# Optimization experiments

Measured on AMD Instinct MI355X. Metric: run time of the kernel, lower is better.

## Reference

```python
import jax, jax.numpy as jnp
import numpy as np

B, S, D, H, DH, BS, L, R, V, FF = 4, 4096, 768, 12, 64, 64, 2, 3, 50257, 3072
NB = S // BS          # 64 key/query blocks
NSEL = 5 + R          # 2 global + 3 window + R random key blocks per query block


def layer_norm(x, g, b, eps=1e-12):
    m = jnp.mean(x, axis=-1, keepdims=True)
    v = jnp.mean(jnp.square(x - m), axis=-1, keepdims=True)
    return (x - m) * jax.lax.rsqrt(v + eps) * g + b


def setup_inputs() -> dict:
    key = jax.random.key(0)
    ks = iter(jax.random.split(key, 16))
    p = lambda shape: jax.random.normal(next(ks), shape, jnp.float32) * 0.02
    return {
        'input_ids': jax.random.randint(next(ks), (B, S), 0, V, jnp.int32),
        'attention_mask': jnp.ones((B, S), jnp.int32),
        'label': jax.random.randint(next(ks), (B,), 0, 2, jnp.int32),
        'rand_idx': jax.random.randint(next(ks), (NB, R), 0, NB, jnp.int32),
        'emb': p((V, D)), 'pos_emb': p((S, D)),
        'ln_emb_g': jnp.ones((D,)), 'ln_emb_b': jnp.zeros((D,)),
        'Wqkv': p((L, D, 3 * D)), 'bqkv': jnp.zeros((L, 3 * D)),
        'Wo': p((L, D, D)), 'bo': jnp.zeros((L, D)),
        'ln1_g': jnp.ones((L, D)), 'ln1_b': jnp.zeros((L, D)),
        'Wff1': p((L, D, FF)), 'bff1': jnp.zeros((L, FF)),
        'Wff2': p((L, FF, D)), 'bff2': jnp.zeros((L, D)),
        'ln2_g': jnp.ones((L, D)), 'ln2_b': jnp.zeros((L, D)),
        'Wp': p((D, D)), 'bp': jnp.zeros((D,)),
        'Wc': p((D, 2)), 'bc': jnp.zeros((2,)),
    }


def reference(input_ids, attention_mask, label, rand_idx, emb, pos_emb,
              ln_emb_g, ln_emb_b, Wqkv, bqkv, Wo, bo, ln1_g, ln1_b,
              Wff1, bff1, Wff2, bff2, ln2_g, ln2_b, Wp, bp, Wc, bc):
    blk = jnp.arange(NB, dtype=jnp.int32)
    sel = jnp.concatenate([
        jnp.zeros((NB, 1), jnp.int32),
        ((blk - 1) % NB)[:, None], blk[:, None], ((blk + 1) % NB)[:, None],
        jnp.full((NB, 1), NB - 1, jnp.int32),
        rand_idx.astype(jnp.int32),
    ], axis=1)  # [NB, NSEL]

    h = emb[input_ids] + pos_emb[None]                 # [B,S,D]
    h = layer_norm(h, ln_emb_g, ln_emb_b)

    mblk = attention_mask.reshape(B, NB, BS)
    mask_sel = mblk[:, sel].reshape(B, 1, NB, 1, NSEL * BS)  # gathered key mask
    bias = jnp.where(mask_sel > 0, 0.0, -1e9).astype(h.dtype)

    scale = 1.0 / np.sqrt(DH)
    for l in range(L):
        qkv = h @ Wqkv[l] + bqkv[l]
        q, k, v = jnp.split(qkv, 3, axis=-1)
        to_blocks = lambda t: t.reshape(B, NB, BS, H, DH).transpose(0, 3, 1, 2, 4)  # [B,H,NB,BS,DH]
        qb, kb, vb = to_blocks(q), to_blocks(k), to_blocks(v)
        ksel = kb[:, :, sel].reshape(B, H, NB, NSEL * BS, DH)  # gather sparse key blocks
        vsel = vb[:, :, sel].reshape(B, H, NB, NSEL * BS, DH)
        scores = jnp.einsum('bhnqd,bhnkd->bhnqk', qb, ksel) * scale + bias
        attn = jax.nn.softmax(scores, axis=-1)
        ob = jnp.einsum('bhnqk,bhnkd->bhnqd', attn, vsel)
        o = ob.transpose(0, 2, 3, 1, 4).reshape(B, S, D)
        h = layer_norm(h + o @ Wo[l] + bo[l], ln1_g[l], ln1_b[l])
        ff = jax.nn.gelu(h @ Wff1[l] + bff1[l]) @ Wff2[l] + bff2[l]
        h = layer_norm(h + ff, ln2_g[l], ln2_b[l])

    pooled = jnp.tanh(h[:, 0] @ Wp + bp)               # BERT-style pooler on [CLS]
    probs = jax.nn.softmax(pooled @ Wc + bc, axis=1)
    # Faithful to the original: CrossEntropyLoss applied to softmax OUTPUT (double softmax)
    loss = -jnp.mean(jax.nn.log_softmax(probs, axis=1)[jnp.arange(B), label])
    return probs, loss
```

## Files before the change

kernel.cpp:

```cpp
#include <hip/hip_runtime.h>
#include <hip/hip_bf16.h>
#include <stdint.h>


using bf16 = __hip_bfloat16;
typedef __bf16 bf16x8 __attribute__((ext_vector_type(8)));
typedef __bf16 bf16x4 __attribute__((ext_vector_type(4)));
typedef float f32x4 __attribute__((ext_vector_type(4)));

__device__ __forceinline__ float b2f(bf16 x) { return __bfloat162float(x); }
__device__ __forceinline__ bf16 f2b(float x) { return __float2bfloat16(x); }
__device__ __forceinline__ __bf16 f2br(float x) {
  bf16 h = __float2bfloat16(x);
  return *reinterpret_cast<__bf16*>(&h);
}
__device__ __forceinline__ float ldf(const void* p, size_t i, int flag) {
  return flag ? __bfloat162float(((const bf16*)p)[i]) : ((const float*)p)[i];
}

__device__ __forceinline__ void gld_lds16(const bf16* g, bf16* l) {
  __builtin_amdgcn_global_load_lds((__attribute__((address_space(1))) void*)g,
                                   (__attribute__((address_space(3))) void*)l, 16, 0, 0);
}

__device__ __forceinline__ f32x4 mfma16(bf16x8 a, bf16x8 b, f32x4 c) {
  return __builtin_amdgcn_mfma_f32_16x16x32_bf16(a, b, c, 0, 0, 0);
}

__device__ __forceinline__ float gelu_f(float x) {
  const float z = 1.5957691216057308f * (x + 0.044715f * x * x * x);
  return x / (1.0f + __expf(-z));
}

__global__ void probe_kernel(const uint32_t* __restrict__ g, int* __restrict__ flag) {
  if (threadIdx.x == 0) flag[0] = (g[0] == 0x3F803F80u) ? 1 : 0;
}

__global__ __launch_bounds__(256) void transpose_k(const void* __restrict__ in, size_t in_off,
                                                   bf16* __restrict__ out, int K, int N,
                                                   const int* __restrict__ dflag) {
  __shared__ float tile[32][33];
  const int flag = dflag[0];
  const int bx = blockIdx.x * 32;
  const int by = blockIdx.y * 32;
  const int tx = threadIdx.x & 31, ty = threadIdx.x >> 5;
#pragma unroll
  for (int i = 0; i < 32; i += 8)
    tile[ty + i][tx] = ldf(in, in_off + (size_t)(by + ty + i) * N + bx + tx, flag);
  __syncthreads();
#pragma unroll
  for (int i = 0; i < 32; i += 8)
    out[(size_t)(bx + ty + i) * K + by + tx] = f2b(tile[tx][ty + i]);
}

__global__ __launch_bounds__(256) void embed_ln_kernel(
    const int* __restrict__ ids, const void* __restrict__ emb, const void* __restrict__ pos,
    const void* __restrict__ g, const void* __restrict__ bb, bf16* __restrict__ h,
    const int* __restrict__ dflag) {
  __shared__ float red[8];
  const int flag = dflag[0];
  const int tok = blockIdx.x;
  const int tid = threadIdx.x;
  const int s = tok & 4095;
  const size_t id = (size_t)ids[tok];
  float v[3]; float sum = 0.f, sq = 0.f;
#pragma unroll
  for (int i = 0; i < 3; i++) {
    const int d = tid + i * 256;
    v[i] = ldf(emb, id * 768 + d, flag) + ldf(pos, (size_t)s * 768 + d, flag);
    sum += v[i]; sq += v[i] * v[i];
  }
#pragma unroll
  for (int off = 32; off >= 1; off >>= 1) { sum += __shfl_down(sum, off); sq += __shfl_down(sq, off); }
  if ((tid & 63) == 0) { red[(tid >> 6) * 2] = sum; red[(tid >> 6) * 2 + 1] = sq; }
  __syncthreads();
  sum = red[0] + red[2] + red[4] + red[6];
  sq  = red[1] + red[3] + red[5] + red[7];
  const float mean = sum * (1.0f / 768.0f);
  const float var = sq * (1.0f / 768.0f) - mean * mean;
  const float rs = rsqrtf(var + 1e-12f);
  bf16* hr = h + (size_t)tok * 768;
#pragma unroll
  for (int i = 0; i < 3; i++) {
    const int d = tid + i * 256;
    hr[d] = f2b((v[i] - mean) * rs * ldf(g, d, flag) + ldf(bb, d, flag));
  }
}

__global__ __launch_bounds__(256) void add_ln_kernel(
    bf16* __restrict__ h, const bf16* __restrict__ x,
    const void* __restrict__ g, const void* __restrict__ bb, size_t goff,
    const int* __restrict__ dflag) {
  __shared__ float red[8];
  const int flag = dflag[0];
  const int tok = blockIdx.x;
  const int tid = threadIdx.x;
  const size_t base = (size_t)tok * 768;
  float v[3]; float sum = 0.f, sq = 0.f;
#pragma unroll
  for (int i = 0; i < 3; i++) {
    const int d = tid + i * 256;
    v[i] = b2f(h[base + d]) + b2f(x[base + d]);
    sum += v[i]; sq += v[i] * v[i];
  }
#pragma unroll
  for (int off = 32; off >= 1; off >>= 1) { sum += __shfl_down(sum, off); sq += __shfl_down(sq, off); }
  if ((tid & 63) == 0) { red[(tid >> 6) * 2] = sum; red[(tid >> 6) * 2 + 1] = sq; }
  __syncthreads();
  sum = red[0] + red[2] + red[4] + red[6];
  sq  = red[1] + red[3] + red[5] + red[7];
  const float mean = sum * (1.0f / 768.0f);
  const float var = sq * (1.0f / 768.0f) - mean * mean;
  const float rs = rsqrtf(var + 1e-12f);
#pragma unroll
  for (int i = 0; i < 3; i++) {
    const int d = tid + i * 256;
    h[base + d] = f2b((v[i] - mean) * rs * ldf(g, goff + d, flag) + ldf(bb, goff + d, flag));
  }
}

template <int EPI, bool ABLK>
__global__ __launch_bounds__(256) void gemm_bt(
    const bf16* __restrict__ A, const bf16* __restrict__ Bt,
    const void* __restrict__ bias, size_t bias_off, bf16* __restrict__ C,
    int N, int K,
    bf16* __restrict__ qout, bf16* __restrict__ kout, bf16* __restrict__ vout,
    const int* __restrict__ dflag) {
  __shared__ __align__(16) bf16 smem[9216];
  bf16* sA = smem;
  bf16* sB = smem + 4096;
  const int m0 = blockIdx.x * 128;
  const int n0 = blockIdx.y * 128;
  const int tid = threadIdx.x;
  const int lane = tid & 63;
  const int wv = tid >> 6;
  const int wm = wv >> 1, wn = wv & 1;
  const int col = lane & 15, quad = lane >> 4;

  f32x4 acc[4][4] = {};

  const int sr = tid >> 2;
  const int kc = ((tid & 3) - ((tid >> 4) & 3)) & 3;
  const int sc = kc * 8;
  const bf16* gA = A + (size_t)(m0 + sr) * K + sc;
  const bf16* gB = Bt + (size_t)(n0 + sr) * K + sc;
  const size_t rstep = (size_t)64 * K;

  size_t cb0 = 0, cb1 = 0;
  if constexpr (ABLK) {
    const int t0 = m0 + sr, t1 = t0 + 64;
    cb0 = (size_t)(t0 >> 12) * 3145728 + ((t0 >> 6) & 63) * 4096 + (t0 & 63) * 64;
    cb1 = (size_t)(t1 >> 12) * 3145728 + ((t1 >> 6) & 63) * 4096 + (t1 & 63) * 64;
  }

  const int sl = (quad + (col >> 2)) & 3;

  for (int k0 = 0; k0 < K; k0 += 32) {
    const bf16 *pA0, *pA1;
    if constexpr (ABLK) {
      const int c = k0 + sc;
      const int hh = c >> 6, dh = c & 63;
      pA0 = A + cb0 + hh * 262144 + dh;
      pA1 = A + cb1 + hh * 262144 + dh;
    } else {
      pA0 = gA; pA1 = gA + rstep; gA += 32;
    }
    gld_lds16(pA0, sA + tid * 8);
    gld_lds16(pA1, sA + 2048 + tid * 8);
    gld_lds16(gB, sB + tid * 8);
    gld_lds16(gB + rstep, sB + 2048 + tid * 8);
    gB += 32;
    __syncthreads();
    bf16x8 av[4], bv[4];
#pragma unroll
    for (int t = 0; t < 4; t++)
      av[t] = *(const bf16x8*)(sA + (wm * 64 + t * 16 + col) * 32 + sl * 8);
#pragma unroll
    for (int t = 0; t < 4; t++)
      bv[t] = *(const bf16x8*)(sB + (wn * 64 + t * 16 + col) * 32 + sl * 8);
#pragma unroll
    for (int mt = 0; mt < 4; mt++)
#pragma unroll
      for (int nt = 0; nt < 4; nt++)
        acc[mt][nt] = mfma16(av[mt], bv[nt], acc[mt][nt]);
    __syncthreads();
  }

  const int flag = dflag[0];
  float bsv[4];
#pragma unroll
  for (int nt = 0; nt < 4; nt++)
    bsv[nt] = ldf(bias, bias_off + n0 + wn * 64 + nt * 16 + col, flag);

  if constexpr (EPI != 2) {
    for (int half = 0; half < 2; half++) {
      __syncthreads();
      if (wm == half) {
#pragma unroll
        for (int nt = 0; nt < 4; nt++)
#pragma unroll
          for (int mt = 0; mt < 4; mt++)
#pragma unroll
            for (int r = 0; r < 4; r++) {
              float val = acc[mt][nt][r] + bsv[nt];
              if constexpr (EPI == 1) val = gelu_f(val);
              smem[(mt * 16 + quad * 4 + r) * 136 + wn * 64 + nt * 16 + col] = f2b(val);
            }
      }
      __syncthreads();
#pragma unroll
      for (int rr = 0; rr < 4; rr++) {
        const int row = rr * 16 + (tid >> 4);
        const int ch = tid & 15;
        const bf16x8 vv = *(const bf16x8*)(smem + row * 136 + ch * 8);
        *(bf16x8*)(C + (size_t)(m0 + half * 64 + row) * N + n0 + ch * 8) = vv;
      }
    }
  } else {
    const int part = (n0 >= 1536) ? 2 : ((n0 >= 768) ? 1 : 0);
    const int w0 = n0 - part * 768;
    const int h0 = w0 >> 6;
    const int bb = m0 >> 12;
    for (int half = 0; half < 2; half++) {
      const int nb_ = ((m0 >> 6) & 63) + half;
      __syncthreads();
      if (wm == half) {
        if (part < 2) {
#pragma unroll
          for (int nt = 0; nt < 4; nt++)
#pragma unroll
            for (int mt = 0; mt < 4; mt++)
#pragma unroll
              for (int r = 0; r < 4; r++)
                smem[(mt * 16 + quad * 4 + r) * 136 + wn * 64 + nt * 16 + col] =
                    f2b(acc[mt][nt][r] + bsv[nt]);
        } else {
#pragma unroll
          for (int nt = 0; nt < 4; nt++) {
            const int ncol = wn * 64 + nt * 16 + col;
#pragma unroll
            for (int mt = 0; mt < 4; mt++) {
              bf16x4 pk;
#pragma unroll
              for (int r = 0; r < 4; r++) pk[r] = f2br(acc[mt][nt][r] + bsv[nt]);
              *(bf16x4*)(smem + ncol * 72 + mt * 16 + quad * 4) = pk;
            }
          }
        }
      }
      __syncthreads();
      const int j = tid >> 7;
      const size_t dbase = (size_t)((bb * 12 + h0 + j) * 64 + nb_) * 4096;
      if (part < 2) {
        bf16* dst = (part == 0) ? qout : kout;
#pragma unroll
        for (int rr = 0; rr < 4; rr++) {
          const int tsk = (tid & 127) + rr * 128;
          const int row = tsk >> 3, pc = tsk & 7;
          const bf16x8 vv = *(const bf16x8*)(smem + row * 136 + j * 64 + pc * 8);
          *(bf16x8*)(dst + dbase + row * 64 + pc * 8) = vv;
        }
      } else {
#pragma unroll
        for (int rr = 0; rr < 4; rr++) {
          const int tsk = (tid & 127) + rr * 128;
          const int dh = tsk >> 3, pc = tsk & 7;
          const bf16x8 vv = *(const bf16x8*)(smem + (j * 64 + dh) * 72 + pc * 8);
          *(bf16x8*)(vout + dbase + dh * 64 + pc * 8) = vv;
        }
      }
    }
  }
}

__global__ __launch_bounds__(256, 4) void attn_kernel(
    const bf16* q, const bf16* __restrict__ kmat, const bf16* __restrict__ vT,
    const int* __restrict__ amask, const int* __restrict__ rand_idx, bf16* o) {
  __shared__ __align__(16) bf16 sK[2][4096];
  __shared__ __align__(16) bf16 sV[2][4096];
  const int idx = blockIdx.x;
  const int nb = idx & 63;
  const int bh = idx >> 6;
  const int bb = bh / 12;
  const int tid = threadIdx.x;
  const int wv = tid >> 6, lane = tid & 63;
  const int col = lane & 15, quad = lane >> 4;

  int sel[8];
  sel[0] = 0; sel[1] = (nb + 63) & 63; sel[2] = nb; sel[3] = (nb + 1) & 63;
  sel[4] = 63;
  sel[5] = rand_idx[nb * 3 + 0];
  sel[6] = rand_idx[nb * 3 + 1];
  sel[7] = rand_idx[nb * 3 + 2];

  const size_t bhbase = (size_t)bh * 64;

  const bf16* qb = q + (bhbase + nb) * 4096;
  const int qrow = wv * 16 + col;
  const bf16x8 bq0 = *(const bf16x8*)(qb + qrow * 64 + quad * 8);
  const bf16x8 bq1 = *(const bf16x8*)(qb + qrow * 64 + 32 + quad * 8);

  unsigned long long bal[8];
#pragma unroll
  for (int sb = 0; sb < 8; sb++)
    bal[sb] = __ballot(amask[bb * 4096 + sel[sb] * 64 + lane] > 0);

  const int srow = tid >> 3, sslot = tid & 7;
  const int sw0 = ((sslot ^ (srow & 7)) << 3);

  auto stage = [&](int buf, int blk) {
    const bf16* gk = kmat + (bhbase + blk) * 4096;
    const bf16* gv = vT + (bhbase + blk) * 4096;
    bf16* dk = sK[buf];
    bf16* dv = sV[buf];
    gld_lds16(gk + srow * 64 + sw0, dk + tid * 8);
    gld_lds16(gk + (srow + 32) * 64 + sw0, dk + 2048 + tid * 8);
    gld_lds16(gv + srow * 64 + sw0, dv + tid * 8);
    gld_lds16(gv + (srow + 32) * 64 + sw0, dv + 2048 + tid * 8);
  };

  f32x4 oacc[4] = {};
  float mrun = -1e30f, lrun = 0.0f;

  stage(0, sel[0]);

#pragma unroll
  for (int sb = 0; sb < 8; sb++) {
    const int cur = sb & 1;
    if (sb < 7) {
      stage(cur ^ 1, sel[sb + 1]);
      asm volatile("s_waitcnt vmcnt(4)" ::: "memory");
    } else {
      asm volatile("s_waitcnt vmcnt(0)" ::: "memory");
    }
    __builtin_amdgcn_s_barrier();
    asm volatile("" ::: "memory");

    const bf16* kb = sK[cur];
    f32x4 t[4];
#pragma unroll
    for (int c = 0; c < 4; c++) {
      const int r = c * 16 + col;
      const bf16x8 ak0 = *(const bf16x8*)(kb + r * 64 + ((quad ^ (r & 7)) << 3));
      const bf16x8 ak1 = *(const bf16x8*)(kb + r * 64 + (((4 + quad) ^ (r & 7)) << 3));
      f32x4 s4 = {};
      s4 = mfma16(ak0, bq0, s4);
      s4 = mfma16(ak1, bq1, s4);
      t[c] = s4;
    }
#pragma unroll
    for (int c = 0; c < 4; c++)
#pragma unroll
      for (int r = 0; r < 4; r++) t[c][r] *= 0.125f;
    if (bal[sb] != ~0ull) {
#pragma unroll
      for (int c = 0; c < 4; c++)
#pragma unroll
        for (int r = 0; r < 4; r++)
          if (!((bal[sb] >> (c * 16 + quad * 4 + r)) & 1)) t[c][r] -= 1e9f;
    }

    float pm = t[0][0];
#pragma unroll
    for (int c = 0; c < 4; c++)
#pragma unroll
      for (int r = 0; r < 4; r++) pm = fmaxf(pm, t[c][r]);
    pm = fmaxf(pm, __shfl_xor(pm, 16));
    pm = fmaxf(pm, __shfl_xor(pm, 32));

    const float mnew = fmaxf(mrun, pm);
    const float scale = __expf(mrun - mnew);
    float ps = 0.0f;
    bf16x8 pa8[2];
#pragma unroll
    for (int c = 0; c < 4; c++)
#pragma unroll
      for (int r = 0; r < 4; r++) {
        const float p = __expf(t[c][r] - mnew);
        ps += p;
        pa8[c >> 1][(c & 1) * 4 + r] = f2br(p);
      }
    ps += __shfl_xor(ps, 16);
    ps += __shfl_xor(ps, 32);
    lrun = lrun * scale + ps;
    mrun = mnew;

    float sc[4];
#pragma unroll
    for (int r = 0; r < 4; r++) sc[r] = __shfl(scale, quad * 4 + r);
#pragma unroll
    for (int nt = 0; nt < 4; nt++)
#pragma unroll
      for (int r = 0; r < 4; r++) oacc[nt][r] *= sc[r];

    const bf16* vb = sV[cur];
#pragma unroll
    for (int pr = 0; pr < 2; pr++) {
      const int g0 = 4 * pr + (quad >> 1);
      const int g1 = g0 + 2;
      const int so = (quad & 1) * 4;
#pragma unroll
      for (int nt = 0; nt < 4; nt++) {
        const int dh = nt * 16 + col;
        const bf16x4 bv0 = *(const bf16x4*)(vb + dh * 64 + ((g0 ^ (col & 7)) << 3) + so);
        const bf16x4 bv1 = *(const bf16x4*)(vb + dh * 64 + ((g1 ^ (col & 7)) << 3) + so);
        const bf16x8 bv8 = __builtin_shufflevector(bv0, bv1, 0, 1, 2, 3, 4, 5, 6, 7);
        oacc[nt] = mfma16(pa8[pr], bv8, oacc[nt]);
      }
    }
    asm volatile("" ::: "memory");
    __builtin_amdgcn_s_barrier();
  }

  const float invl = 1.0f / lrun;
  float iv[4];
#pragma unroll
  for (int r = 0; r < 4; r++) iv[r] = __shfl(invl, quad * 4 + r);
  bf16* ob = o + (bhbase + nb) * 4096;
#pragma unroll
  for (int nt = 0; nt < 4; nt++)
#pragma unroll
    for (int r = 0; r < 4; r++)
      ob[(wv * 16 + quad * 4 + r) * 64 + nt * 16 + col] = f2b(oacc[nt][r] * iv[r]);
}

__global__ __launch_bounds__(768) void pooler_kernel(
    const bf16* __restrict__ h, const void* __restrict__ Wp,
    const void* __restrict__ bp, float* __restrict__ pooled,
    const int* __restrict__ dflag) {
  __shared__ float hrow[768];
  const int flag = dflag[0];
  const int bb = blockIdx.x;
  const int j = threadIdx.x;
  hrow[j] = b2f(h[(size_t)bb * 4096 * 768 + j]);
  __syncthreads();
  float acc = 0.0f;
#pragma unroll 8
  for (int d = 0; d < 768; d++) acc += hrow[d] * ldf(Wp, (size_t)d * 768 + j, flag);
  pooled[bb * 768 + j] = tanhf(acc + ldf(bp, j, flag));
}

__global__ __launch_bounds__(256) void cls_kernel(
    const float* __restrict__ pooled, const void* __restrict__ Wc, const void* __restrict__ bc,
    const int* __restrict__ label, void* __restrict__ out, const int* __restrict__ dflag) {
  __shared__ float lsum[8];
  const int flag = dflag[0];
  const int tid = threadIdx.x;
  const int p = tid >> 5, i = tid & 31;
  const int bb = p >> 1, c = p & 1;
  float acc = 0.0f;
  for (int d = i; d < 768; d += 32) acc += pooled[bb * 768 + d] * ldf(Wc, (size_t)d * 2 + c, flag);
#pragma unroll
  for (int off = 16; off >= 1; off >>= 1) acc += __shfl_xor(acc, off);
  if (i == 0) lsum[p] = acc;
  __syncthreads();
  if (tid == 0) {
    float res[9];
    float loss = 0.0f;
    for (int b = 0; b < 4; b++) {
      const float l0 = lsum[b * 2 + 0] + ldf(bc, 0, flag);
      const float l1 = lsum[b * 2 + 1] + ldf(bc, 1, flag);
      const float m = fmaxf(l0, l1);
      const float e0 = expf(l0 - m), e1 = expf(l1 - m);
      const float s = e0 + e1;
      const float p0 = e0 / s, p1 = e1 / s;
      res[b * 2] = p0; res[b * 2 + 1] = p1;
      const float mm = fmaxf(p0, p1);
      const float lse = mm + logf(expf(p0 - mm) + expf(p1 - mm));
      const float chosen = (label[b] == 0) ? p0 : p1;
      loss -= (chosen - lse);
    }
    res[8] = loss * 0.25f;
    if (flag) { bf16* o = (bf16*)out; for (int j = 0; j < 9; j++) o[j] = f2b(res[j]); }
    else      { float* o = (float*)out; for (int j = 0; j < 9; j++) o[j] = res[j]; }
  }
}

extern "C" void kernel_launch(void* const* d_in, const int* in_sizes, int n_in,
                              void* d_out, int out_size, void* d_ws, size_t ws_size,
                              hipStream_t stream) {
  const int* input_ids      = (const int*)d_in[0];
  const int* attention_mask = (const int*)d_in[1];
  const int* label          = (const int*)d_in[2];
  const int* rand_idx       = (const int*)d_in[3];
  const void* emb      = d_in[4];
  const void* pos_emb  = d_in[5];
  const void* ln_emb_g = d_in[6];
  const void* ln_emb_b = d_in[7];
  const void* Wqkv = d_in[8];
  const void* bqkv = d_in[9];
  const void* Wo   = d_in[10];
  const void* bo   = d_in[11];
  const void* ln1_g = d_in[12];
  const void* ln1_b = d_in[13];
  const void* Wff1 = d_in[14];
  const void* bff1 = d_in[15];
  const void* Wff2 = d_in[16];
  const void* bff2 = d_in[17];
  const void* ln2_g = d_in[18];
  const void* ln2_b = d_in[19];
  const void* Wp = d_in[20];
  const void* bp = d_in[21];
  const void* Wc = d_in[22];
  const void* bc = d_in[23];

  bf16* ws = (bf16*)d_ws;
  size_t off = 0;
  int* dflag = (int*)(ws + off); off += 8;
  bf16* WqkvT = ws + off; off += (size_t)2 * 2304 * 768;
  bf16* WoT   = ws + off; off += (size_t)2 * 768 * 768;
  bf16* Wff1T = ws + off; off += (size_t)2 * 3072 * 768;
  bf16* Wff2T = ws + off; off += (size_t)2 * 768 * 3072;
  bf16* hbuf  = ws + off; off += (size_t)16384 * 768;
  bf16* qo    = ws + off; off += (size_t)16384 * 768;
  bf16* kbf   = ws + off; off += (size_t)16384 * 768;
  bf16* vbf   = ws + off; off += (size_t)16384 * 768;
  bf16* xbf   = ws + off; off += (size_t)16384 * 768;
  bf16* a1buf = ws + off; off += (size_t)16384 * 3072;
  float* pooled = (float*)(ws + off); off += 6144;

  dim3 blk(256);

  probe_kernel<<<1, 64, 0, stream>>>((const uint32_t*)ln_emb_g, dflag);

  for (int l = 0; l < 2; l++) {
    transpose_k<<<dim3(72, 24), blk, 0, stream>>>(Wqkv, (size_t)l * 768 * 2304, WqkvT + (size_t)l * 2304 * 768, 768, 2304, dflag);
    transpose_k<<<dim3(24, 24), blk, 0, stream>>>(Wo, (size_t)l * 768 * 768, WoT + (size_t)l * 768 * 768, 768, 768, dflag);
    transpose_k<<<dim3(96, 24), blk, 0, stream>>>(Wff1, (size_t)l * 768 * 3072, Wff1T + (size_t)l * 3072 * 768, 768, 3072, dflag);
    transpose_k<<<dim3(24, 96), blk, 0, stream>>>(Wff2, (size_t)l * 3072 * 768, Wff2T + (size_t)l * 768 * 3072, 3072, 768, dflag);
  }

  embed_ln_kernel<<<16384, blk, 0, stream>>>(input_ids, emb, pos_emb, ln_emb_g, ln_emb_b, hbuf, dflag);

  for (int l = 0; l < 2; l++) {
    gemm_bt<2, false><<<dim3(128, 18), blk, 0, stream>>>(hbuf, WqkvT + (size_t)l * 2304 * 768, bqkv, (size_t)l * 2304,
                                                         nullptr, 2304, 768, qo, kbf, vbf, dflag);
    attn_kernel<<<3072, blk, 0, stream>>>(qo, kbf, vbf, attention_mask, rand_idx, qo);
    gemm_bt<0, true><<<dim3(128, 6), blk, 0, stream>>>(qo, WoT + (size_t)l * 768 * 768, bo, (size_t)l * 768,
                                                       xbf, 768, 768, nullptr, nullptr, nullptr, dflag);
    add_ln_kernel<<<16384, blk, 0, stream>>>(hbuf, xbf, ln1_g, ln1_b, (size_t)l * 768, dflag);
    gemm_bt<1, false><<<dim3(128, 24), blk, 0, stream>>>(hbuf, Wff1T + (size_t)l * 3072 * 768, bff1, (size_t)l * 3072,
                                                         a1buf, 3072, 768, nullptr, nullptr, nullptr, dflag);
    gemm_bt<0, false><<<dim3(128, 6), blk, 0, stream>>>(a1buf, Wff2T + (size_t)l * 768 * 3072, bff2, (size_t)l * 768,
                                                        xbf, 768, 3072, nullptr, nullptr, nullptr, dflag);
    add_ln_kernel<<<16384, blk, 0, stream>>>(hbuf, xbf, ln2_g, ln2_b, (size_t)l * 768, dflag);
  }

  pooler_kernel<<<4, dim3(768), 0, stream>>>(hbuf, Wp, bp, pooled, dflag);
  cls_kernel<<<1, blk, 0, stream>>>(pooled, Wc, bc, label, d_out, dflag);

  (void)in_sizes; (void)n_in; (void)out_size; (void)ws_size;
}
```

Measured before the change: 1.545 ms.

## Double-buffer GEMM LDS staging and make add-LayerNorm one wave per token

The GEMM main loop now keeps two LDS buffers and issues the global-to-LDS loads for the next K-slice before computing the current one. It uses partial vmcnt waits and raw barriers, so memory latency can overlap with the MFMAs. Separately, the residual-add LayerNorm kernel processes one token per wavefront with 16-byte vector loads and stores and a pure shuffle reduction, removing the shared-memory reduction and block barrier. The costs are doubled LDS per GEMM block, which may reduce occupancy, and hand-written waitcnt logic that must match the exact number of outstanding loads.

```diff
diff --git a/kernel.cpp b/kernel.cpp
--- a/kernel.cpp
+++ b/kernel.cpp
@@ -13,6 +13,9 @@
 __device__ __forceinline__ __bf16 f2br(float x) {
   bf16 h = __float2bfloat16(x);
   return *reinterpret_cast<__bf16*>(&h);
+}
+__device__ __forceinline__ float br2f(__bf16 x) {
+  bf16 t; *reinterpret_cast<__bf16*>(&t) = x; return __bfloat162float(t);
 }
 __device__ __forceinline__ float ldf(const void* p, size_t i, int flag) {
   return flag ? __bfloat162float(((const bf16*)p)[i]) : ((const float*)p)[i];
@@ -91,31 +94,51 @@
     bf16* __restrict__ h, const bf16* __restrict__ x,
     const void* __restrict__ g, const void* __restrict__ bb, size_t goff,
     const int* __restrict__ dflag) {
-  __shared__ float red[8];
   const int flag = dflag[0];
-  const int tok = blockIdx.x;
   const int tid = threadIdx.x;
+  const int wv = tid >> 6, lane = tid & 63;
+  const int tok = blockIdx.x * 4 + wv;
   const size_t base = (size_t)tok * 768;
-  float v[3]; float sum = 0.f, sq = 0.f;
-#pragma unroll
-  for (int i = 0; i < 3; i++) {
-    const int d = tid + i * 256;
-    v[i] = b2f(h[base + d]) + b2f(x[base + d]);
-    sum += v[i]; sq += v[i] * v[i];
-  }
-#pragma unroll
-  for (int off = 32; off >= 1; off >>= 1) { sum += __shfl_down(sum, off); sq += __shfl_down(sq, off); }
-  if ((tid & 63) == 0) { red[(tid >> 6) * 2] = sum; red[(tid >> 6) * 2 + 1] = sq; }
-  __syncthreads();
-  sum = red[0] + red[2] + red[4] + red[6];
-  sq  = red[1] + red[3] + red[5] + red[7];
+
+  float v[16];
+  float sum = 0.f, sq = 0.f;
+  const bf16x8 h0 = *(const bf16x8*)(h + base + lane * 8);
+  const bf16x8 x0 = *(const bf16x8*)(x + base + lane * 8);
+#pragma unroll
+  for (int j = 0; j < 8; j++) {
+    const float t = br2f(h0[j]) + br2f(x0[j]);
+    v[j] = t; sum += t; sq += t * t;
+  }
+  if (lane < 32) {
+    const bf16x8 h1 = *(const bf16x8*)(h + base + 512 + lane * 8);
+    const bf16x8 x1 = *(const bf16x8*)(x + base + 512 + lane * 8);
+#pragma unroll
+    for (int j = 0; j < 8; j++) {
+      const float t = br2f(h1[j]) + br2f(x1[j]);
+      v[8 + j] = t; sum += t; sq += t * t;
+    }
+  }
+#pragma unroll
+  for (int off = 32; off >= 1; off >>= 1) { sum += __shfl_xor(sum, off); sq += __shfl_xor(sq, off); }
   const float mean = sum * (1.0f / 768.0f);
   const float var = sq * (1.0f / 768.0f) - mean * mean;
   const float rs = rsqrtf(var + 1e-12f);
-#pragma unroll
-  for (int i = 0; i < 3; i++) {
-    const int d = tid + i * 256;
-    h[base + d] = f2b((v[i] - mean) * rs * ldf(g, goff + d, flag) + ldf(bb, goff + d, flag));
+
+  bf16x8 o0;
+#pragma unroll
+  for (int j = 0; j < 8; j++) {
+    const int d = lane * 8 + j;
+    o0[j] = f2br((v[j] - mean) * rs * ldf(g, goff + d, flag) + ldf(bb, goff + d, flag));
+  }
+  *(bf16x8*)(h + base + lane * 8) = o0;
+  if (lane < 32) {
+    bf16x8 o1;
+#pragma unroll
+    for (int j = 0; j < 8; j++) {
+      const int d = 512 + lane * 8 + j;
+      o1[j] = f2br((v[8 + j] - mean) * rs * ldf(g, goff + d, flag) + ldf(bb, goff + d, flag));
+    }
+    *(bf16x8*)(h + base + 512 + lane * 8) = o1;
   }
 }
 
@@ -126,9 +149,7 @@
     int N, int K,
     bf16* __restrict__ qout, bf16* __restrict__ kout, bf16* __restrict__ vout,
     const int* __restrict__ dflag) {
-  __shared__ __align__(16) bf16 smem[9216];
-  bf16* sA = smem;
-  bf16* sB = smem + 4096;
+  __shared__ __align__(16) bf16 smem[16384];
   const int m0 = blockIdx.x * 128;
   const int n0 = blockIdx.y * 128;
   const int tid = threadIdx.x;
@@ -155,35 +176,55 @@
 
   const int sl = (quad + (col >> 2)) & 3;
 
-  for (int k0 = 0; k0 < K; k0 += 32) {
+  auto stage = [&](int buf, int kk) {
+    bf16* dA = smem + buf * 8192;
+    bf16* dB = dA + 4096;
     const bf16 *pA0, *pA1;
     if constexpr (ABLK) {
-      const int c = k0 + sc;
+      const int c = kk + sc;
       const int hh = c >> 6, dh = c & 63;
       pA0 = A + cb0 + hh * 262144 + dh;
       pA1 = A + cb1 + hh * 262144 + dh;
     } else {
-      pA0 = gA; pA1 = gA + rstep; gA += 32;
-    }
-    gld_lds16(pA0, sA + tid * 8);
-    gld_lds16(pA1, sA + 2048 + tid * 8);
-    gld_lds16(gB, sB + tid * 8);
-    gld_lds16(gB + rstep, sB + 2048 + tid * 8);
-    gB += 32;
-    __syncthreads();
+      pA0 = gA + kk; pA1 = gA + rstep + kk;
+    }
+    gld_lds16(pA0, dA + tid * 8);
+    gld_lds16(pA1, dA + 2048 + tid * 8);
+    gld_lds16(gB + kk, dB + tid * 8);
+    gld_lds16(gB + rstep + kk, dB + 2048 + tid * 8);
+  };
+
+  const int nIter = K >> 5;
+  stage(0, 0);
+
+  for (int it = 0; it < nIter; ++it) {
+    const int cur = it & 1;
+    if (it + 1 < nIter) {
+      stage(cur ^ 1, (it + 1) * 32);
+      asm volatile("s_waitcnt vmcnt(4)" ::: "memory");
+    } else {
+      asm volatile("s_waitcnt vmcnt(0)" ::: "memory");
+    }
+    __builtin_amdgcn_s_barrier();
+    asm volatile("" ::: "memory");
+
+    const bf16* cA = smem + cur * 8192;
+    const bf16* cB = cA + 4096;
     bf16x8 av[4], bv[4];
 #pragma unroll
     for (int t = 0; t < 4; t++)
-      av[t] = *(const bf16x8*)(sA + (wm * 64 + t * 16 + col) * 32 + sl * 8);
+      av[t] = *(const bf16x8*)(cA + (wm * 64 + t * 16 + col) * 32 + sl * 8);
 #pragma unroll
     for (int t = 0; t < 4; t++)
-      bv[t] = *(const bf16x8*)(sB + (wn * 64 + t * 16 + col) * 32 + sl * 8);
+      bv[t] = *(const bf16x8*)(cB + (wn * 64 + t * 16 + col) * 32 + sl * 8);
 #pragma unroll
     for (int mt = 0; mt < 4; mt++)
 #pragma unroll
       for (int nt = 0; nt < 4; nt++)
         acc[mt][nt] = mfma16(av[mt], bv[nt], acc[mt][nt]);
-    __syncthreads();
+
+    asm volatile("" ::: "memory");
+    __builtin_amdgcn_s_barrier();
   }
 
   const int flag = dflag[0];
@@ -538,12 +579,12 @@
     attn_kernel<<<3072, blk, 0, stream>>>(qo, kbf, vbf, attention_mask, rand_idx, qo);
     gemm_bt<0, true><<<dim3(128, 6), blk, 0, stream>>>(qo, WoT + (size_t)l * 768 * 768, bo, (size_t)l * 768,
                                                        xbf, 768, 768, nullptr, nullptr, nullptr, dflag);
-    add_ln_kernel<<<16384, blk, 0, stream>>>(hbuf, xbf, ln1_g, ln1_b, (size_t)l * 768, dflag);
+    add_ln_kernel<<<4096, blk, 0, stream>>>(hbuf, xbf, ln1_g, ln1_b, (size_t)l * 768, dflag);
     gemm_bt<1, false><<<dim3(128, 24), blk, 0, stream>>>(hbuf, Wff1T + (size_t)l * 3072 * 768, bff1, (size_t)l * 3072,
                                                          a1buf, 3072, 768, nullptr, nullptr, nullptr, dflag);
     gemm_bt<0, false><<<dim3(128, 6), blk, 0, stream>>>(a1buf, Wff2T + (size_t)l * 768 * 3072, bff2, (size_t)l * 768,
                                                         xbf, 768, 3072, nullptr, nullptr, nullptr, dflag);
-    add_ln_kernel<<<16384, blk, 0, stream>>>(hbuf, xbf, ln2_g, ln2_b, (size_t)l * 768, dflag);
+    add_ln_kernel<<<4096, blk, 0, stream>>>(hbuf, xbf, ln2_g, ln2_b, (size_t)l * 768, dflag);
   }
 
   pooler_kernel<<<4, dim3(768), 0, stream>>>(hbuf, Wp, bp, pooled, dflag);
```

Result: no change. 1.572 ms (+1.7%).
